# Kernel optimization log

Hardware: AMD Instinct MI355X
Metric: run time of the kernel (lower is better)

## Reference

```python
import jax, jax.numpy as jnp
import numpy as np

IN_DIM = 256
QK_DIM = IN_DIM // 8


def setup_inputs() -> dict:
    key = jax.random.key(0)
    ks = jax.random.split(key, 10)
    B, C, W, H = 4, IN_DIM, 64, 64
    a = jax.random.normal(ks[0], (B, C, W, H), dtype=jnp.float32)
    b = jax.random.normal(ks[1], (B, C, W, H), dtype=jnp.float32)
    c = jax.random.uniform(ks[2], (B, 1, 2 * W, 2 * H), dtype=jnp.float32)
    scale = 0.02
    wq = jax.random.normal(ks[3], (QK_DIM, C), dtype=jnp.float32) * scale
    bq = jnp.zeros((QK_DIM,), dtype=jnp.float32)
    wk = jax.random.normal(ks[4], (QK_DIM, C), dtype=jnp.float32) * scale
    bk = jnp.zeros((QK_DIM,), dtype=jnp.float32)
    wv = jax.random.normal(ks[5], (C, C), dtype=jnp.float32) * scale
    bv = jnp.zeros((C,), dtype=jnp.float32)
    gamma = jnp.ones((1,), dtype=jnp.float32)
    return {"a": a, "b": b, "c": c, "wq": wq, "bq": bq, "wk": wk,
            "bk": bk, "wv": wv, "bv": bv, "gamma": gamma}


def reference(a, b, c, wq, bq, wk, bk, wv, bv, gamma):
    B, C, W, H = a.shape
    N = W * H
    # F.interpolate(c, scale_factor=1/down_rate, mode='nearest'): output idx i -> input idx i*down_rate
    down = c.shape[2] // W
    cd = c[:, :, ::down, ::down]                      # [B,1,W,H]
    # 1x1 convs as channel contractions
    q = jnp.einsum('bchw,oc->bohw', a, wq) + bq[None, :, None, None]
    k = jnp.einsum('bchw,oc->bohw', b, wk) + bk[None, :, None, None]
    v = jnp.einsum('bchw,oc->bohw', a, wv) + bv[None, :, None, None]
    qf = q.reshape(B, QK_DIM, N)                      # proj_query^T rows are spatial
    kf = k.reshape(B, QK_DIM, N)
    vf = v.reshape(B, C, N)
    sim = jnp.einsum('bdi,bdj->bij', qf, kf)          # [B,N,N]
    cflat = cd.reshape(B, N)
    # mask[b,i,j] = cflat[b,i] (per-query multiplicative logit scaling)
    logits = sim * cflat[:, :, None]
    attn = jax.nn.softmax(logits, axis=-1)            # [B,N,N]
    out_attn = jnp.einsum('bcj,bij->bci', vf, attn).reshape(B, C, W, H)
    out = gamma * a * cd + (1.0 - cd) * out_attn
    return out
```

## Files before the change

kernel.cpp:

```cpp
#include <hip/hip_runtime.h>

#define LOG2E 1.44269504088896340736f

typedef __attribute__((ext_vector_type(8))) short short8;
typedef __attribute__((ext_vector_type(4))) float float4v;
typedef __attribute__((ext_vector_type(2))) float float2v;
typedef __attribute__((ext_vector_type(2))) int int2v;
typedef __attribute__((ext_vector_type(4))) int int4v;

__device__ inline unsigned short f2bf(float f) {
    union { float f; unsigned u; } v; v.f = f;
    unsigned r = v.u + 0x7fffu + ((v.u >> 16) & 1u);
    return (unsigned short)(r >> 16);
}
__device__ inline float bf2f(unsigned short u) {
    union { unsigned u; float f; } v; v.u = ((unsigned)u) << 16;
    return v.f;
}
__device__ inline unsigned pk_bf16(float a, float b) {
    union { float f; unsigned u; } ua, ub; ua.f = a; ub.f = b;
    return __builtin_amdgcn_perm(ub.u + 0x8000u, ua.u + 0x8000u, 0x07060302u);
}

__global__ void wcvt_kernel(const float* __restrict__ wq, const float* __restrict__ wk,
                            const float* __restrict__ wv, unsigned short* __restrict__ Wbf)
{
    int idx = blockIdx.x * 256 + threadIdx.x;
    int e4  = idx * 4;
    int row = e4 >> 8, col = e4 & 255;
    const float* src = (row < 32) ? (wq + row * 256 + col)
                     : (row < 64) ? (wk + (row - 32) * 256 + col)
                                  : (wv + (row - 64) * 256 + col);
    float4v v = *(const float4v*)src;
    int2v p;
    p.x = (unsigned)f2bf(v[0]) | ((unsigned)f2bf(v[1]) << 16);
    p.y = (unsigned)f2bf(v[2]) | ((unsigned)f2bf(v[3]) << 16);
    *(int2v*)(Wbf + e4) = p;
}

__launch_bounds__(512, 2)
__global__ void proj_kernel(const float* __restrict__ a_p, const float* __restrict__ b_p,
                            const float* __restrict__ c_p,
                            const float* __restrict__ bq, const float* __restrict__ bk,
                            const float* __restrict__ bv,
                            const unsigned short* __restrict__ Wbf,
                            unsigned short* __restrict__ Qg, unsigned short* __restrict__ Kg,
                            unsigned short* __restrict__ Vg)
{
    __shared__ __align__(16) unsigned short At[64 * 264];
    __shared__ __align__(16) unsigned short Bt[64 * 264];
    __shared__ float bias[320];
    __shared__ float cdl[64];

    const int t    = threadIdx.x;
    const int blk  = blockIdx.x;
    const int b    = blk & 3;
    const int tile = blk >> 2;
    const int i0   = tile * 64;
    const int lane = t & 63;
    const int w    = t >> 6;
    const int q    = lane >> 4;
    const int n    = lane & 15;
    const int it   = w & 3;
    const int mh   = w >> 2;

    {
        const int arr = t >> 8, cp = (t >> 1) & 127, ih = (t & 1) * 32;
        const float* src = (arr ? b_p : a_p) + ((size_t)(b * 256 + 2 * cp)) * 4096 + i0 + ih;
        unsigned* dst = (unsigned*)(arr ? Bt : At) + cp;
#pragma unroll
        for (int h = 0; h < 4; ++h) {
            float4v r0a = *(const float4v*)(src + h * 8);
            float4v r0b = *(const float4v*)(src + h * 8 + 4);
            float4v r1a = *(const float4v*)(src + 4096 + h * 8);
            float4v r1b = *(const float4v*)(src + 4096 + h * 8 + 4);
#pragma unroll
            for (int jj = 0; jj < 4; ++jj)
                dst[(ih + h * 8 + jj) * 132] = pk_bf16(r0a[jj], r1a[jj]);
#pragma unroll
            for (int jj = 0; jj < 4; ++jj)
                dst[(ih + h * 8 + 4 + jj) * 132] = pk_bf16(r0b[jj], r1b[jj]);
        }
        if (t < 320) bias[t] = (t < 32) ? bq[t] : (t < 64) ? bk[t - 32] : bv[t - 64];
        else if (t < 384) cdl[t - 320] = c_p[b * 16384 + tile * 256 + (t - 320) * 2];
    }
    __syncthreads();

    float4v acc[10];
#pragma unroll
    for (int j = 0; j < 10; ++j) acc[j] = (float4v){0.f, 0.f, 0.f, 0.f};

#pragma unroll 2
    for (int kc = 0; kc < 8; ++kc) {
        short8 xa = *(const short8*)&At[(it * 16 + n) * 264 + kc * 32 + q * 8];
        short8 xb = xa;
        if (mh == 0)
            xb = *(const short8*)&Bt[(it * 16 + n) * 264 + kc * 32 + q * 8];
#pragma unroll
        for (int j = 0; j < 10; ++j) {
            int mt = mh * 10 + j;
            short8 wf = *(const short8*)(Wbf + (size_t)(mt * 16 + n) * 256 + kc * 32 + q * 8);
            short8 bsel = (mt == 2 || mt == 3) ? xb : xa;
            acc[j] = __builtin_amdgcn_mfma_f32_16x16x32_bf16(wf, bsel, acc[j], 0, 0, 0);
        }
    }
    __syncthreads();

    unsigned short* QKst = At;
    unsigned short* Vst  = Bt;
    {
        const float cdq = cdl[it * 16 + n] * LOG2E;
#pragma unroll
        for (int j = 0; j < 10; ++j) {
            int mt = mh * 10 + j;
            float4v bv4 = *(const float4v*)&bias[mt * 16 + q * 4];
            float v0 = acc[j][0] + bv4[0], v1 = acc[j][1] + bv4[1];
            float v2 = acc[j][2] + bv4[2], v3 = acc[j][3] + bv4[3];
            if (mt < 2) {
                v0 *= cdq; v1 *= cdq; v2 *= cdq; v3 *= cdq;
                int2v pk; pk.x = (int)pk_bf16(v0, v1); pk.y = (int)pk_bf16(v2, v3);
                *(int2v*)&QKst[(it * 16 + n) * 72 + mt * 16 + q * 4] = pk;
            } else if (mt < 4) {
                int2v pk; pk.x = (int)pk_bf16(v0, v1); pk.y = (int)pk_bf16(v2, v3);
                *(int2v*)&QKst[(it * 16 + n) * 72 + mt * 16 + q * 4] = pk;
            } else {
                int p = ((n >> 2) * 8) + ((it & 1) * 4) + (n & 3);
                int cbase = mt * 16 - 64 + q * 4;
                int jb = it >> 1;
                Vst[((jb * 256) + cbase + 0) * 32 + p] = f2bf(v0);
                Vst[((jb * 256) + cbase + 1) * 32 + p] = f2bf(v1);
                Vst[((jb * 256) + cbase + 2) * 32 + p] = f2bf(v2);
                Vst[((jb * 256) + cbase + 3) * 32 + p] = f2bf(v3);
            }
        }
    }
    __syncthreads();

    {
        int i = t >> 3, h8 = t & 7;
        int4v v = *(const int4v*)&QKst[i * 72 + h8 * 8];
        unsigned short* dstp = (h8 < 4)
            ? Qg + (size_t)(b * 4096 + i0 + i) * 32 + h8 * 8
            : Kg + (size_t)(b * 4096 + i0 + i) * 32 + (h8 - 4) * 8;
        *(int4v*)dstp = v;
    }
    {
#pragma unroll
        for (int k = 0; k < 4; ++k) {
            int flat = k * 512 + t;
            int4v v = *(const int4v*)&Vst[flat * 8];
            int jb = flat >> 10;
            *(int4v*)(Vg + (size_t)(b * 128 + tile * 2 + jb) * 8192 + (flat & 1023) * 8) = v;
        }
    }
}

__launch_bounds__(512, 2)
__global__ void attn_kernel(const unsigned short* __restrict__ Qg,
                            const unsigned short* __restrict__ Kg,
                            const unsigned short* __restrict__ Vg,
                            const float* __restrict__ a_p, const float* __restrict__ c_p,
                            const float* __restrict__ gamma_p, float* __restrict__ out)
{
    __shared__ unsigned short Obuf[256 * 68];
    __shared__ float Lb0[64], Lb1[64], cdl[64];

    const int t    = threadIdx.x;
    const int blk  = blockIdx.x;
    const int b    = blk & 3;
    const int rt   = blk >> 2;
    const int i0   = rt * 64;
    const int lane = t & 63;
    const int w    = t >> 6;
    const int q    = lane >> 4;
    const int n    = lane & 15;
    const int cs   = w & 3;
    const int h    = w >> 2;

    if (t < 64) cdl[t] = c_p[b * 16384 + rt * 256 + t * 2];

    short8 qf[4];
#pragma unroll
    for (int ig = 0; ig < 4; ++ig)
        qf[ig] = *(const short8*)(Qg + (size_t)(b * 4096 + i0 + ig * 16 + n) * 32 + q * 8);

    float4v acc[4][4];
#pragma unroll
    for (int ig = 0; ig < 4; ++ig)
#pragma unroll
        for (int ct = 0; ct < 4; ++ct) acc[ig][ct] = (float4v){0.f, 0.f, 0.f, 0.f};
    float lsc[4] = {0.f, 0.f, 0.f, 0.f};

    const float4v m16v = (float4v){-16.f, -16.f, -16.f, -16.f};

    const unsigned short* kb = Kg + (size_t)(b * 4096 + h * 2048 + n) * 32 + q * 8;
    const unsigned short* vb = Vg + ((size_t)((b * 128 + h * 64) * 256 + cs * 64 + n)) * 32 + q * 8;

    short8 kf0 = *(const short8*)(kb);
    short8 kf1 = *(const short8*)(kb + 512);

#pragma unroll 1
    for (int it = 0; it < 64; ++it) {
        short8 vf[4];
#pragma unroll
        for (int ct = 0; ct < 4; ++ct)
            vf[ct] = *(const short8*)(vb + ct * 512);

        short8 pf[4];
#pragma unroll
        for (int ig = 0; ig < 4; ++ig) {
            float4v s0 = __builtin_amdgcn_mfma_f32_16x16x32_bf16(kf0, qf[ig], m16v, 0, 0, 0);
            float4v s1 = __builtin_amdgcn_mfma_f32_16x16x32_bf16(kf1, qf[ig], m16v, 0, 0, 0);
            float p0 = __builtin_amdgcn_exp2f(s0[0]), p1 = __builtin_amdgcn_exp2f(s0[1]);
            float p2 = __builtin_amdgcn_exp2f(s0[2]), p3 = __builtin_amdgcn_exp2f(s0[3]);
            float p4 = __builtin_amdgcn_exp2f(s1[0]), p5 = __builtin_amdgcn_exp2f(s1[1]);
            float p6 = __builtin_amdgcn_exp2f(s1[2]), p7 = __builtin_amdgcn_exp2f(s1[3]);
            lsc[ig] += ((p0 + p1) + (p2 + p3)) + ((p4 + p5) + (p6 + p7));
            union { short8 s8; unsigned u[4]; } pf_;
            pf_.u[0] = pk_bf16(p0, p1);
            pf_.u[1] = pk_bf16(p2, p3);
            pf_.u[2] = pk_bf16(p4, p5);
            pf_.u[3] = pk_bf16(p6, p7);
            pf[ig] = pf_.s8;
        }

        kf0 = *(const short8*)(kb + 1024);
        kf1 = *(const short8*)(kb + 1536);

#pragma unroll
        for (int ig = 0; ig < 4; ++ig)
#pragma unroll
            for (int ct = 0; ct < 4; ++ct)
                acc[ig][ct] = __builtin_amdgcn_mfma_f32_16x16x32_bf16(pf[ig], vf[ct], acc[ig][ct], 0, 0, 0);

        kb += 1024;
        vb += 8192;
    }

    float lred[4];
#pragma unroll
    for (int ig = 0; ig < 4; ++ig) {
        float v = lsc[ig];
        v += __shfl_xor(v, 16, 64);
        v += __shfl_xor(v, 32, 64);
        lred[ig] = v;
    }
    {
        const int cbase = cs * 64;
        const int ct0 = h ? 0 : 2;
#pragma unroll
        for (int ig = 0; ig < 4; ++ig)
#pragma unroll
            for (int cc = 0; cc < 2; ++cc) {
                int ct = ct0 + cc;
                int c = cbase + ct * 16 + n;
                int i = ig * 16 + q * 4;
                int2v pk;
                pk.x = (int)pk_bf16(acc[ig][ct][0], acc[ig][ct][1]);
                pk.y = (int)pk_bf16(acc[ig][ct][2], acc[ig][ct][3]);
                *(int2v*)&Obuf[c * 68 + i] = pk;
            }
        if (w == 0) {
#pragma unroll
            for (int ig = 0; ig < 4; ++ig) if (lane < 16) Lb0[ig * 16 + lane] = lred[ig];
        } else if (w == 4) {
#pragma unroll
            for (int ig = 0; ig < 4; ++ig) if (lane < 16) Lb1[ig * 16 + lane] = lred[ig];
        }
    }
    __syncthreads();
    {
        const int cbase = cs * 64;
        const int ctf = h ? 2 : 0;
        const float gam = gamma_p[0];
#pragma unroll
        for (int ig = 0; ig < 4; ++ig) {
            int ib = ig * 16 + q * 4;
            float invL[4], cdv[4];
#pragma unroll
            for (int r = 0; r < 4; ++r) {
                invL[r] = 1.0f / (Lb0[ib + r] + Lb1[ib + r]);
                cdv[r]  = cdl[ib + r];
            }
#pragma unroll
            for (int cc = 0; cc < 2; ++cc) {
                int ct = ctf + cc;
                int c = cbase + ct * 16 + n;
                int2v st = *(const int2v*)&Obuf[c * 68 + ib];
                size_t gi = ((size_t)(b * 256 + c)) * 4096 + i0 + ib;
                float4v av = *(const float4v*)(a_p + gi);
                float4v ov;
#pragma unroll
                for (int r = 0; r < 4; ++r) {
                    unsigned pr = (r < 2) ? (unsigned)st.x : (unsigned)st.y;
                    float part = bf2f((unsigned short)((r & 1) ? (pr >> 16) : (pr & 0xffffu)));
                    float o = (acc[ig][ct][r] + part) * invL[r];
                    ov[r] = gam * av[r] * cdv[r] + (1.0f - cdv[r]) * o;
                }
                *(float4v*)(out + gi) = ov;
            }
        }
    }
}

extern "C" void kernel_launch(void* const* d_in, const int* in_sizes, int n_in,
                              void* d_out, int out_size, void* d_ws, size_t ws_size,
                              hipStream_t stream)
{
    const float* a_p   = (const float*)d_in[0];
    const float* b_p   = (const float*)d_in[1];
    const float* c_p   = (const float*)d_in[2];
    const float* wq    = (const float*)d_in[3];
    const float* bq    = (const float*)d_in[4];
    const float* wk    = (const float*)d_in[5];
    const float* bk    = (const float*)d_in[6];
    const float* wv    = (const float*)d_in[7];
    const float* bv    = (const float*)d_in[8];
    const float* gamma = (const float*)d_in[9];
    float* out = (float*)d_out;

    unsigned short* Qg  = (unsigned short*)d_ws;
    unsigned short* Kg  = Qg + (size_t)4 * 4096 * 32;
    unsigned short* Vg  = Kg + (size_t)4 * 4096 * 32;
    unsigned short* Wbf = Vg + (size_t)4 * 256 * 4096;

    wcvt_kernel<<<80, 256, 0, stream>>>(wq, wk, wv, Wbf);
    proj_kernel<<<256, 512, 0, stream>>>(a_p, b_p, c_p, bq, bk, bv, Wbf, Qg, Kg, Vg);
    attn_kernel<<<256, 512, 0, stream>>>(Qg, Kg, Vg, a_p, c_p, gamma, out);
}
```

Baseline: 195.5 us.

## Halve row tiles to 32 and double grid size for projection and attention

Both the projection and attention kernels now work on 32-row spatial tiles instead of 64, so each launches 512 blocks instead of 256. Launch bounds rise to 4 blocks per SM, and per-thread accumulators and LDS staging shrink to match. With 256 blocks the grid roughly matched the CU count of 256 on MI355X; doubling it is meant to improve load balance and latency hiding. The attention epilogue now writes both half-sum partials to separate LDS buffers and combines them in a cooperative pass, at the cost of re-reading K and V twice as often across blocks.

```diff
diff --git a/kernel.cpp b/kernel.cpp
--- a/kernel.cpp
+++ b/kernel.cpp
@@ -38,7 +38,7 @@
     *(int2v*)(Wbf + e4) = p;
 }
 
-__launch_bounds__(512, 2)
+__launch_bounds__(512, 4)
 __global__ void proj_kernel(const float* __restrict__ a_p, const float* __restrict__ b_p,
                             const float* __restrict__ c_p,
                             const float* __restrict__ bq, const float* __restrict__ bk,
@@ -47,29 +47,32 @@
                             unsigned short* __restrict__ Qg, unsigned short* __restrict__ Kg,
                             unsigned short* __restrict__ Vg)
 {
-    __shared__ __align__(16) unsigned short At[64 * 264];
-    __shared__ __align__(16) unsigned short Bt[64 * 264];
+    __shared__ __align__(16) unsigned short At[32 * 264];
+    __shared__ __align__(16) unsigned short Bt[32 * 264];
     __shared__ float bias[320];
-    __shared__ float cdl[64];
+    __shared__ float cdl[32];
 
     const int t    = threadIdx.x;
     const int blk  = blockIdx.x;
     const int b    = blk & 3;
     const int tile = blk >> 2;
-    const int i0   = tile * 64;
+    const int i0   = tile * 32;
     const int lane = t & 63;
     const int w    = t >> 6;
     const int q    = lane >> 4;
     const int n    = lane & 15;
-    const int it   = w & 3;
-    const int mh   = w >> 2;
-
-    {
-        const int arr = t >> 8, cp = (t >> 1) & 127, ih = (t & 1) * 32;
+    const int it   = w & 1;
+    const int mh   = w >> 1;
+
+    {
+        const int arr = t >> 8;
+        const int tt  = t & 255;
+        const int cp  = tt >> 1;
+        const int ih  = (tt & 1) * 16;
         const float* src = (arr ? b_p : a_p) + ((size_t)(b * 256 + 2 * cp)) * 4096 + i0 + ih;
         unsigned* dst = (unsigned*)(arr ? Bt : At) + cp;
 #pragma unroll
-        for (int h = 0; h < 4; ++h) {
+        for (int h = 0; h < 2; ++h) {
             float4v r0a = *(const float4v*)(src + h * 8);
             float4v r0b = *(const float4v*)(src + h * 8 + 4);
             float4v r1a = *(const float4v*)(src + 4096 + h * 8);
@@ -82,13 +85,16 @@
                 dst[(ih + h * 8 + 4 + jj) * 132] = pk_bf16(r0b[jj], r1b[jj]);
         }
         if (t < 320) bias[t] = (t < 32) ? bq[t] : (t < 64) ? bk[t - 32] : bv[t - 64];
-        else if (t < 384) cdl[t - 320] = c_p[b * 16384 + tile * 256 + (t - 320) * 2];
+        else if (t < 352) {
+            int u = t - 320;
+            cdl[u] = c_p[b * 16384 + (tile >> 1) * 256 + (tile & 1) * 64 + u * 2];
+        }
     }
     __syncthreads();
 
-    float4v acc[10];
-#pragma unroll
-    for (int j = 0; j < 10; ++j) acc[j] = (float4v){0.f, 0.f, 0.f, 0.f};
+    float4v acc[5];
+#pragma unroll
+    for (int j = 0; j < 5; ++j) acc[j] = (float4v){0.f, 0.f, 0.f, 0.f};
 
 #pragma unroll 2
     for (int kc = 0; kc < 8; ++kc) {
@@ -97,8 +103,8 @@
         if (mh == 0)
             xb = *(const short8*)&Bt[(it * 16 + n) * 264 + kc * 32 + q * 8];
 #pragma unroll
-        for (int j = 0; j < 10; ++j) {
-            int mt = mh * 10 + j;
+        for (int j = 0; j < 5; ++j) {
+            int mt = mh * 5 + j;
             short8 wf = *(const short8*)(Wbf + (size_t)(mt * 16 + n) * 256 + kc * 32 + q * 8);
             short8 bsel = (mt == 2 || mt == 3) ? xb : xa;
             acc[j] = __builtin_amdgcn_mfma_f32_16x16x32_bf16(wf, bsel, acc[j], 0, 0, 0);
@@ -111,8 +117,8 @@
     {
         const float cdq = cdl[it * 16 + n] * LOG2E;
 #pragma unroll
-        for (int j = 0; j < 10; ++j) {
-            int mt = mh * 10 + j;
+        for (int j = 0; j < 5; ++j) {
+            int mt = mh * 5 + j;
             float4v bv4 = *(const float4v*)&bias[mt * 16 + q * 4];
             float v0 = acc[j][0] + bv4[0], v1 = acc[j][1] + bv4[1];
             float v2 = acc[j][2] + bv4[2], v3 = acc[j][3] + bv4[3];
@@ -126,17 +132,16 @@
             } else {
                 int p = ((n >> 2) * 8) + ((it & 1) * 4) + (n & 3);
                 int cbase = mt * 16 - 64 + q * 4;
-                int jb = it >> 1;
-                Vst[((jb * 256) + cbase + 0) * 32 + p] = f2bf(v0);
-                Vst[((jb * 256) + cbase + 1) * 32 + p] = f2bf(v1);
-                Vst[((jb * 256) + cbase + 2) * 32 + p] = f2bf(v2);
-                Vst[((jb * 256) + cbase + 3) * 32 + p] = f2bf(v3);
+                Vst[(cbase + 0) * 32 + p] = f2bf(v0);
+                Vst[(cbase + 1) * 32 + p] = f2bf(v1);
+                Vst[(cbase + 2) * 32 + p] = f2bf(v2);
+                Vst[(cbase + 3) * 32 + p] = f2bf(v3);
             }
         }
     }
     __syncthreads();
 
-    {
+    if (t < 256) {
         int i = t >> 3, h8 = t & 7;
         int4v v = *(const int4v*)&QKst[i * 72 + h8 * 8];
         unsigned short* dstp = (h8 < 4)
@@ -146,30 +151,30 @@
     }
     {
 #pragma unroll
-        for (int k = 0; k < 4; ++k) {
+        for (int k = 0; k < 2; ++k) {
             int flat = k * 512 + t;
             int4v v = *(const int4v*)&Vst[flat * 8];
-            int jb = flat >> 10;
-            *(int4v*)(Vg + (size_t)(b * 128 + tile * 2 + jb) * 8192 + (flat & 1023) * 8) = v;
-        }
-    }
-}
-
-__launch_bounds__(512, 2)
+            *(int4v*)(Vg + (size_t)(b * 128 + tile) * 8192 + (size_t)flat * 8) = v;
+        }
+    }
+}
+
+__launch_bounds__(512, 4)
 __global__ void attn_kernel(const unsigned short* __restrict__ Qg,
                             const unsigned short* __restrict__ Kg,
                             const unsigned short* __restrict__ Vg,
                             const float* __restrict__ a_p, const float* __restrict__ c_p,
                             const float* __restrict__ gamma_p, float* __restrict__ out)
 {
-    __shared__ unsigned short Obuf[256 * 68];
-    __shared__ float Lb0[64], Lb1[64], cdl[64];
+    __shared__ unsigned short ObufA[256 * 36];
+    __shared__ unsigned short ObufB[256 * 36];
+    __shared__ float Lb0[32], Lb1[32], cdl[32];
 
     const int t    = threadIdx.x;
     const int blk  = blockIdx.x;
     const int b    = blk & 3;
     const int rt   = blk >> 2;
-    const int i0   = rt * 64;
+    const int i0   = rt * 32;
     const int lane = t & 63;
     const int w    = t >> 6;
     const int q    = lane >> 4;
@@ -177,19 +182,19 @@
     const int cs   = w & 3;
     const int h    = w >> 2;
 
-    if (t < 64) cdl[t] = c_p[b * 16384 + rt * 256 + t * 2];
-
-    short8 qf[4];
-#pragma unroll
-    for (int ig = 0; ig < 4; ++ig)
+    if (t < 32) cdl[t] = c_p[b * 16384 + (rt >> 1) * 256 + (rt & 1) * 64 + t * 2];
+
+    short8 qf[2];
+#pragma unroll
+    for (int ig = 0; ig < 2; ++ig)
         qf[ig] = *(const short8*)(Qg + (size_t)(b * 4096 + i0 + ig * 16 + n) * 32 + q * 8);
 
-    float4v acc[4][4];
-#pragma unroll
-    for (int ig = 0; ig < 4; ++ig)
+    float4v acc[2][4];
+#pragma unroll
+    for (int ig = 0; ig < 2; ++ig)
 #pragma unroll
         for (int ct = 0; ct < 4; ++ct) acc[ig][ct] = (float4v){0.f, 0.f, 0.f, 0.f};
-    float lsc[4] = {0.f, 0.f, 0.f, 0.f};
+    float lsc[2] = {0.f, 0.f};
 
     const float4v m16v = (float4v){-16.f, -16.f, -16.f, -16.f};
 
@@ -206,9 +211,9 @@
         for (int ct = 0; ct < 4; ++ct)
             vf[ct] = *(const short8*)(vb + ct * 512);
 
-        short8 pf[4];
-#pragma unroll
-        for (int ig = 0; ig < 4; ++ig) {
+        short8 pf[2];
+#pragma unroll
+        for (int ig = 0; ig < 2; ++ig) {
             float4v s0 = __builtin_amdgcn_mfma_f32_16x16x32_bf16(kf0, qf[ig], m16v, 0, 0, 0);
             float4v s1 = __builtin_amdgcn_mfma_f32_16x16x32_bf16(kf1, qf[ig], m16v, 0, 0, 0);
             float p0 = __builtin_amdgcn_exp2f(s0[0]), p1 = __builtin_amdgcn_exp2f(s0[1]);
@@ -228,7 +233,7 @@
         kf1 = *(const short8*)(kb + 1536);
 
 #pragma unroll
-        for (int ig = 0; ig < 4; ++ig)
+        for (int ig = 0; ig < 2; ++ig)
 #pragma unroll
             for (int ct = 0; ct < 4; ++ct)
                 acc[ig][ct] = __builtin_amdgcn_mfma_f32_16x16x32_bf16(pf[ig], vf[ct], acc[ig][ct], 0, 0, 0);
@@ -237,68 +242,62 @@
         vb += 8192;
     }
 
-    float lred[4];
-#pragma unroll
-    for (int ig = 0; ig < 4; ++ig) {
+    float lred[2];
+#pragma unroll
+    for (int ig = 0; ig < 2; ++ig) {
         float v = lsc[ig];
         v += __shfl_xor(v, 16, 64);
         v += __shfl_xor(v, 32, 64);
         lred[ig] = v;
     }
     {
-        const int cbase = cs * 64;
-        const int ct0 = h ? 0 : 2;
-#pragma unroll
-        for (int ig = 0; ig < 4; ++ig)
-#pragma unroll
-            for (int cc = 0; cc < 2; ++cc) {
-                int ct = ct0 + cc;
-                int c = cbase + ct * 16 + n;
-                int i = ig * 16 + q * 4;
+        unsigned short* Ob = h ? ObufB : ObufA;
+#pragma unroll
+        for (int ig = 0; ig < 2; ++ig)
+#pragma unroll
+            for (int ct = 0; ct < 4; ++ct) {
+                int c = cs * 64 + ct * 16 + n;
                 int2v pk;
                 pk.x = (int)pk_bf16(acc[ig][ct][0], acc[ig][ct][1]);
                 pk.y = (int)pk_bf16(acc[ig][ct][2], acc[ig][ct][3]);
-                *(int2v*)&Obuf[c * 68 + i] = pk;
+                *(int2v*)&Ob[c * 36 + ig * 16 + q * 4] = pk;
             }
         if (w == 0) {
-#pragma unroll
-            for (int ig = 0; ig < 4; ++ig) if (lane < 16) Lb0[ig * 16 + lane] = lred[ig];
+            if (lane < 16) { Lb0[lane] = lred[0]; Lb0[16 + lane] = lred[1]; }
         } else if (w == 4) {
-#pragma unroll
-            for (int ig = 0; ig < 4; ++ig) if (lane < 16) Lb1[ig * 16 + lane] = lred[ig];
+            if (lane < 16) { Lb1[lane] = lred[0]; Lb1[16 + lane] = lred[1]; }
         }
     }
     __syncthreads();
-    {
-        const int cbase = cs * 64;
-        const int ctf = h ? 2 : 0;
+
+    {
         const float gam = gamma_p[0];
-#pragma unroll
-        for (int ig = 0; ig < 4; ++ig) {
-            int ib = ig * 16 + q * 4;
-            float invL[4], cdv[4];
+        const int e = t & 7;
+        float invL[4], cdv[4];
+#pragma unroll
+        for (int r = 0; r < 4; ++r) {
+            int i = e * 4 + r;
+            invL[r] = 1.0f / (Lb0[i] + Lb1[i]);
+            cdv[r]  = cdl[i];
+        }
+#pragma unroll
+        for (int k = 0; k < 4; ++k) {
+            int c = k * 64 + (t >> 3);
+            int2v pa = *(const int2v*)&ObufA[c * 36 + e * 4];
+            int2v pb = *(const int2v*)&ObufB[c * 36 + e * 4];
+            size_t gi = ((size_t)(b * 256 + c)) * 4096 + i0 + e * 4;
+            float4v av = *(const float4v*)(a_p + gi);
+            float4v ov;
 #pragma unroll
             for (int r = 0; r < 4; ++r) {
-                invL[r] = 1.0f / (Lb0[ib + r] + Lb1[ib + r]);
-                cdv[r]  = cdl[ib + r];
+                unsigned wa = (r < 2) ? (unsigned)pa.x : (unsigned)pa.y;
+                unsigned wb = (r < 2) ? (unsigned)pb.x : (unsigned)pb.y;
+                float oa = bf2f((unsigned short)((r & 1) ? (wa >> 16) : (wa & 0xffffu)));
+                float ob = bf2f((unsigned short)((r & 1) ? (wb >> 16) : (wb & 0xffffu)));
+                float o = (oa + ob) * invL[r];
+                ov[r] = gam * av[r] * cdv[r] + (1.0f - cdv[r]) * o;
             }
-#pragma unroll
-            for (int cc = 0; cc < 2; ++cc) {
-                int ct = ctf + cc;
-                int c = cbase + ct * 16 + n;
-                int2v st = *(const int2v*)&Obuf[c * 68 + ib];
-                size_t gi = ((size_t)(b * 256 + c)) * 4096 + i0 + ib;
-                float4v av = *(const float4v*)(a_p + gi);
-                float4v ov;
-#pragma unroll
-                for (int r = 0; r < 4; ++r) {
-                    unsigned pr = (r < 2) ? (unsigned)st.x : (unsigned)st.y;
-                    float part = bf2f((unsigned short)((r & 1) ? (pr >> 16) : (pr & 0xffffu)));
-                    float o = (acc[ig][ct][r] + part) * invL[r];
-                    ov[r] = gam * av[r] * cdv[r] + (1.0f - cdv[r]) * o;
-                }
-                *(float4v*)(out + gi) = ov;
-            }
+            *(float4v*)(out + gi) = ov;
         }
     }
 }
@@ -325,6 +324,6 @@
     unsigned short* Wbf = Vg + (size_t)4 * 256 * 4096;
 
     wcvt_kernel<<<80, 256, 0, stream>>>(wq, wk, wv, Wbf);
-    proj_kernel<<<256, 512, 0, stream>>>(a_p, b_p, c_p, bq, bk, bv, Wbf, Qg, Kg, Vg);
-    attn_kernel<<<256, 512, 0, stream>>>(Qg, Kg, Vg, a_p, c_p, gamma, out);
-}
+    proj_kernel<<<512, 512, 0, stream>>>(a_p, b_p, c_p, bq, bk, bv, Wbf, Qg, Kg, Vg);
+    attn_kernel<<<512, 512, 0, stream>>>(Qg, Kg, Vg, a_p, c_p, gamma, out);
+}
```

After: 206.7 us. +5.8%, slower.

## Split attention key range across four wave groups and recoalesce projection staging

Applied to the files above, without the earlier changes.

The attention kernel now launches 1024 threads per block, splitting the key dimension into four quarters instead of two. Each quarter writes its partial bf16 output to its own shared buffer, and a separate epilogue sums the four partials with a thread mapping that gives coalesced output stores. The projection kernel's staging loop is remapped to coalesced float4 loads, and the LDS row stride is padded to 266 to cut bank conflicts. The cost is higher LDS use (four 34KB buffers), a launch bound of four waves per SIMD that caps registers per thread, and an extra bf16 rounding in the partial sums.

```diff
diff --git a/kernel.cpp b/kernel.cpp
--- a/kernel.cpp
+++ b/kernel.cpp
@@ -47,8 +47,8 @@
                             unsigned short* __restrict__ Qg, unsigned short* __restrict__ Kg,
                             unsigned short* __restrict__ Vg)
 {
-    __shared__ __align__(16) unsigned short At[64 * 264];
-    __shared__ __align__(16) unsigned short Bt[64 * 264];
+    __shared__ __align__(16) unsigned short At[64 * 266];
+    __shared__ __align__(16) unsigned short Bt[64 * 266];
     __shared__ float bias[320];
     __shared__ float cdl[64];
 
@@ -65,21 +65,19 @@
     const int mh   = w >> 2;
 
     {
-        const int arr = t >> 8, cp = (t >> 1) & 127, ih = (t & 1) * 32;
-        const float* src = (arr ? b_p : a_p) + ((size_t)(b * 256 + 2 * cp)) * 4096 + i0 + ih;
-        unsigned* dst = (unsigned*)(arr ? Bt : At) + cp;
-#pragma unroll
-        for (int h = 0; h < 4; ++h) {
-            float4v r0a = *(const float4v*)(src + h * 8);
-            float4v r0b = *(const float4v*)(src + h * 8 + 4);
-            float4v r1a = *(const float4v*)(src + 4096 + h * 8);
-            float4v r1b = *(const float4v*)(src + 4096 + h * 8 + 4);
-#pragma unroll
-            for (int jj = 0; jj < 4; ++jj)
-                dst[(ih + h * 8 + jj) * 132] = pk_bf16(r0a[jj], r1a[jj]);
-#pragma unroll
-            for (int jj = 0; jj < 4; ++jj)
-                dst[(ih + h * 8 + 4 + jj) * 132] = pk_bf16(r0b[jj], r1b[jj]);
+        const int arr = t >> 8, tt = t & 255;
+        unsigned* dst = (unsigned*)(arr ? Bt : At);
+        const float* base = (arr ? b_p : a_p) + (size_t)b * 256 * 4096 + i0;
+#pragma unroll
+        for (int r = 0; r < 8; ++r) {
+            int task = r * 256 + tt;
+            int cp = task >> 4, px4 = (task & 15) * 4;
+            const float* s0 = base + (size_t)(2 * cp) * 4096 + px4;
+            float4v r0 = *(const float4v*)s0;
+            float4v r1 = *(const float4v*)(s0 + 4096);
+#pragma unroll
+            for (int k = 0; k < 4; ++k)
+                dst[(px4 + k) * 133 + cp] = pk_bf16(r0[k], r1[k]);
         }
         if (t < 320) bias[t] = (t < 32) ? bq[t] : (t < 64) ? bk[t - 32] : bv[t - 64];
         else if (t < 384) cdl[t - 320] = c_p[b * 16384 + tile * 256 + (t - 320) * 2];
@@ -92,10 +90,10 @@
 
 #pragma unroll 2
     for (int kc = 0; kc < 8; ++kc) {
-        short8 xa = *(const short8*)&At[(it * 16 + n) * 264 + kc * 32 + q * 8];
+        short8 xa = *(const short8*)&At[(it * 16 + n) * 266 + kc * 32 + q * 8];
         short8 xb = xa;
         if (mh == 0)
-            xb = *(const short8*)&Bt[(it * 16 + n) * 264 + kc * 32 + q * 8];
+            xb = *(const short8*)&Bt[(it * 16 + n) * 266 + kc * 32 + q * 8];
 #pragma unroll
         for (int j = 0; j < 10; ++j) {
             int mt = mh * 10 + j;
@@ -155,15 +153,16 @@
     }
 }
 
-__launch_bounds__(512, 2)
+__launch_bounds__(1024, 4)
 __global__ void attn_kernel(const unsigned short* __restrict__ Qg,
                             const unsigned short* __restrict__ Kg,
                             const unsigned short* __restrict__ Vg,
                             const float* __restrict__ a_p, const float* __restrict__ c_p,
                             const float* __restrict__ gamma_p, float* __restrict__ out)
 {
-    __shared__ unsigned short Obuf[256 * 68];
-    __shared__ float Lb0[64], Lb1[64], cdl[64];
+    __shared__ unsigned short Obuf[4][256 * 68];
+    __shared__ float Lb[4][64];
+    __shared__ float cdl[64];
 
     const int t    = threadIdx.x;
     const int blk  = blockIdx.x;
@@ -175,7 +174,7 @@
     const int q    = lane >> 4;
     const int n    = lane & 15;
     const int cs   = w & 3;
-    const int h    = w >> 2;
+    const int hq   = w >> 2;
 
     if (t < 64) cdl[t] = c_p[b * 16384 + rt * 256 + t * 2];
 
@@ -193,14 +192,14 @@
 
     const float4v m16v = (float4v){-16.f, -16.f, -16.f, -16.f};
 
-    const unsigned short* kb = Kg + (size_t)(b * 4096 + h * 2048 + n) * 32 + q * 8;
-    const unsigned short* vb = Vg + ((size_t)((b * 128 + h * 64) * 256 + cs * 64 + n)) * 32 + q * 8;
+    const unsigned short* kb = Kg + (size_t)(b * 4096 + hq * 1024 + n) * 32 + q * 8;
+    const unsigned short* vb = Vg + ((size_t)((b * 128 + hq * 32) * 256 + cs * 64 + n)) * 32 + q * 8;
 
     short8 kf0 = *(const short8*)(kb);
     short8 kf1 = *(const short8*)(kb + 512);
 
 #pragma unroll 1
-    for (int it = 0; it < 64; ++it) {
+    for (int it = 0; it < 32; ++it) {
         short8 vf[4];
 #pragma unroll
         for (int ct = 0; ct < 4; ++ct)
@@ -246,59 +245,56 @@
         lred[ig] = v;
     }
     {
-        const int cbase = cs * 64;
-        const int ct0 = h ? 0 : 2;
+        unsigned short* Ob = &Obuf[hq][0];
 #pragma unroll
         for (int ig = 0; ig < 4; ++ig)
 #pragma unroll
-            for (int cc = 0; cc < 2; ++cc) {
-                int ct = ct0 + cc;
-                int c = cbase + ct * 16 + n;
-                int i = ig * 16 + q * 4;
+            for (int ct = 0; ct < 4; ++ct) {
+                int c = cs * 64 + ct * 16 + n;
                 int2v pk;
                 pk.x = (int)pk_bf16(acc[ig][ct][0], acc[ig][ct][1]);
                 pk.y = (int)pk_bf16(acc[ig][ct][2], acc[ig][ct][3]);
-                *(int2v*)&Obuf[c * 68 + i] = pk;
+                *(int2v*)&Ob[c * 68 + ig * 16 + q * 4] = pk;
             }
-        if (w == 0) {
-#pragma unroll
-            for (int ig = 0; ig < 4; ++ig) if (lane < 16) Lb0[ig * 16 + lane] = lred[ig];
-        } else if (w == 4) {
-#pragma unroll
-            for (int ig = 0; ig < 4; ++ig) if (lane < 16) Lb1[ig * 16 + lane] = lred[ig];
+        if (cs == 0 && lane < 16) {
+#pragma unroll
+            for (int ig = 0; ig < 4; ++ig) Lb[hq][ig * 16 + lane] = lred[ig];
         }
     }
     __syncthreads();
-    {
-        const int cbase = cs * 64;
-        const int ctf = h ? 2 : 0;
+
+    {
         const float gam = gamma_p[0];
-#pragma unroll
-        for (int ig = 0; ig < 4; ++ig) {
-            int ib = ig * 16 + q * 4;
-            float invL[4], cdv[4];
-#pragma unroll
-            for (int r = 0; r < 4; ++r) {
-                invL[r] = 1.0f / (Lb0[ib + r] + Lb1[ib + r]);
-                cdv[r]  = cdl[ib + r];
+        const int e = t & 15;
+        const int crow = t >> 4;
+        float invL[4], cdv[4];
+#pragma unroll
+        for (int r = 0; r < 4; ++r) {
+            int i = e * 4 + r;
+            invL[r] = 1.0f / (Lb[0][i] + Lb[1][i] + Lb[2][i] + Lb[3][i]);
+            cdv[r]  = cdl[i];
+        }
+#pragma unroll
+        for (int k = 0; k < 4; ++k) {
+            int c = k * 64 + crow;
+            float o0 = 0.f, o1 = 0.f, o2 = 0.f, o3 = 0.f;
+#pragma unroll
+            for (int s = 0; s < 4; ++s) {
+                int2v p = *(const int2v*)&Obuf[s][c * 68 + e * 4];
+                unsigned x = (unsigned)p.x, y = (unsigned)p.y;
+                o0 += bf2f((unsigned short)(x & 0xffffu));
+                o1 += bf2f((unsigned short)(x >> 16));
+                o2 += bf2f((unsigned short)(y & 0xffffu));
+                o3 += bf2f((unsigned short)(y >> 16));
             }
-#pragma unroll
-            for (int cc = 0; cc < 2; ++cc) {
-                int ct = ctf + cc;
-                int c = cbase + ct * 16 + n;
-                int2v st = *(const int2v*)&Obuf[c * 68 + ib];
-                size_t gi = ((size_t)(b * 256 + c)) * 4096 + i0 + ib;
-                float4v av = *(const float4v*)(a_p + gi);
-                float4v ov;
-#pragma unroll
-                for (int r = 0; r < 4; ++r) {
-                    unsigned pr = (r < 2) ? (unsigned)st.x : (unsigned)st.y;
-                    float part = bf2f((unsigned short)((r & 1) ? (pr >> 16) : (pr & 0xffffu)));
-                    float o = (acc[ig][ct][r] + part) * invL[r];
-                    ov[r] = gam * av[r] * cdv[r] + (1.0f - cdv[r]) * o;
-                }
-                *(float4v*)(out + gi) = ov;
-            }
+            size_t gi = ((size_t)(b * 256 + c)) * 4096 + i0 + e * 4;
+            float4v av = *(const float4v*)(a_p + gi);
+            float4v ov;
+            ov[0] = gam * av[0] * cdv[0] + (1.0f - cdv[0]) * (o0 * invL[0]);
+            ov[1] = gam * av[1] * cdv[1] + (1.0f - cdv[1]) * (o1 * invL[1]);
+            ov[2] = gam * av[2] * cdv[2] + (1.0f - cdv[2]) * (o2 * invL[2]);
+            ov[3] = gam * av[3] * cdv[3] + (1.0f - cdv[3]) * (o3 * invL[3]);
+            *(float4v*)(out + gi) = ov;
         }
     }
 }
@@ -326,5 +322,5 @@
 
     wcvt_kernel<<<80, 256, 0, stream>>>(wq, wk, wv, Wbf);
     proj_kernel<<<256, 512, 0, stream>>>(a_p, b_p, c_p, bq, bk, bv, Wbf, Qg, Kg, Vg);
-    attn_kernel<<<256, 512, 0, stream>>>(Qg, Kg, Vg, a_p, c_p, gamma, out);
-}
+    attn_kernel<<<256, 1024, 0, stream>>>(Qg, Kg, Vg, a_p, c_p, gamma, out);
+}
```

After: 277.2 us. +41.8%, slower.
